# Optimization experiments

Measured on AMD Instinct MI355X. Metric: run time of the kernel, lower is better.

## Reference

```python
import jax, jax.numpy as jnp
import numpy as np

N_NODES = 50000
N_EDGES = 800000
H_DIM = 64
N_RELS = 8
N_BASES = 2
N_LAYERS = 2


def setup_inputs() -> dict:
    key = jax.random.key(0)
    ks = jax.random.split(key, 10)
    scale = 1.0 / np.sqrt(H_DIM)
    features = jax.random.normal(ks[0], (N_NODES, H_DIM), dtype=jnp.float32)
    src = jax.random.randint(ks[1], (N_EDGES,), 0, N_NODES, dtype=jnp.int32)
    dst = jax.random.randint(ks[2], (N_EDGES,), 0, N_NODES, dtype=jnp.int32)
    etype = jax.random.randint(ks[3], (N_EDGES,), 0, N_RELS, dtype=jnp.int32)
    # basis weights V: [L, B, H, H], coefficients comp: [L, R, B]
    V = jax.random.normal(ks[4], (N_LAYERS, N_BASES, H_DIM, H_DIM), dtype=jnp.float32) * scale
    comp = jax.random.normal(ks[5], (N_LAYERS, N_RELS, N_BASES), dtype=jnp.float32)
    loop_w = jax.random.normal(ks[6], (N_LAYERS, H_DIM, H_DIM), dtype=jnp.float32) * scale
    layer_bias = jnp.zeros((N_LAYERS, H_DIM), dtype=jnp.float32)
    fc_w = jax.random.normal(ks[7], (1, N_NODES * H_DIM), dtype=jnp.float32) * (1.0 / np.sqrt(N_NODES * H_DIM))
    fc_b = jnp.zeros((1,), dtype=jnp.float32)
    return {
        "features": features, "V": V, "comp": comp, "loop_w": loop_w,
        "layer_bias": layer_bias, "fc_w": fc_w, "fc_b": fc_b,
        "src": src, "dst": dst, "etype": etype,
    }


def reference(features, V, comp, loop_w, layer_bias, fc_w, fc_b, src, dst, etype):
    N, H = features.shape
    L = V.shape[0]
    x = features
    for l in range(L):
        # basis decomposition: project nodes through each basis first (N*B*H, cheap),
        # then mix per-edge with relation coefficients -> avoids per-edge [H,H] weights
        proj = jnp.einsum('ni,bio->nbo', x, V[l])          # [N, B, H]
        msg = jnp.einsum('eb,ebo->eo', comp[l][etype], proj[src])  # [E, H]
        agg = jax.ops.segment_sum(msg, dst, num_segments=N)        # [N, H]
        h = agg + x @ loop_w[l] + layer_bias[l]
        x = jax.nn.relu(h) if l < L - 1 else h
    flat = x.reshape(1, -1)                                # [1, N*H]
    return jax.nn.sigmoid(flat @ fc_w.T + fc_b)            # [1, 1]
```

## Files before the change

### kernel.cpp

```cpp
#include <hip/hip_runtime.h>
#include <hip/hip_bf16.h>
#include <math.h>

#define N_NODES 50000
#define N_EDGES 800000
#define HDIM 64

#define NBUCKET 98
#define BSHIFT  9
#define BCAP    10240

typedef short bf16x8 __attribute__((ext_vector_type(8)));
typedef float f32x4  __attribute__((ext_vector_type(4)));
typedef unsigned short ushort_t;

__device__ __forceinline__ ushort_t f2bf(float f) {
    __hip_bfloat16 b = __float2bfloat16(f);
    return *(ushort_t*)&b;
}
__device__ __forceinline__ void unpack8(uint4 u, float* f) {
    f[0] = __uint_as_float(u.x << 16); f[1] = __uint_as_float(u.x & 0xFFFF0000u);
    f[2] = __uint_as_float(u.y << 16); f[3] = __uint_as_float(u.y & 0xFFFF0000u);
    f[4] = __uint_as_float(u.z << 16); f[5] = __uint_as_float(u.z & 0xFFFF0000u);
    f[6] = __uint_as_float(u.w << 16); f[7] = __uint_as_float(u.w & 0xFFFF0000u);
}

__global__ __launch_bounds__(256) void prep_kernel(
    const float* __restrict__ features, ushort_t* __restrict__ x_bf,
    const float* __restrict__ V, const float* __restrict__ lw,
    ushort_t* __restrict__ Wt, int* __restrict__ bucketFill,
    float* __restrict__ scalar)
{
    const int b = blockIdx.x;
    const int t = threadIdx.x;
    if (b < 3125) {
        const int i = b * 256 + t;
        const float4 v = ((const float4*)features)[i];
        ushort4 o = { f2bf(v.x), f2bf(v.y), f2bf(v.z), f2bf(v.w) };
        *(ushort4*)&x_bf[(size_t)i * 4] = o;
    } else if (b < 3221) {
        const int e = (b - 3125) * 256 + t;
        const int l = e / 12288, r = e % 12288;
        const int n = r / 192, k = r % 192;
        const int sel = k >> 6, i = k & 63;
        const float val = (sel < 2) ? V[l * 8192 + sel * 4096 + i * 64 + n]
                                    : lw[l * 4096 + i * 64 + n];
        Wt[e] = f2bf(val);
    } else {
        if (t < NBUCKET) bucketFill[t] = 0;
        if (t == NBUCKET) scalar[0] = 0.0f;
    }
}

__global__ __launch_bounds__(256) void bucket_scatter(
    const int* __restrict__ src, const int* __restrict__ dst,
    const int* __restrict__ etype, int* __restrict__ bucketFill,
    unsigned int* __restrict__ buf)
{
    __shared__ int cnt[NBUCKET];
    __shared__ int base[NBUCKET];
    const int t = threadIdx.x;
    if (t < NBUCKET) cnt[t] = 0;
    __syncthreads();

    int rank[8], bkt[8];
    unsigned pay[8];
    bool valid[8];
#pragma unroll
    for (int k = 0; k < 8; ++k) {
        const int e = blockIdx.x * 2048 + k * 256 + t;
        valid[k] = (e < N_EDGES);
        if (valid[k]) {
            const int d = dst[e];
            const int b = d >> BSHIFT;
            bkt[k] = b;
            pay[k] = (unsigned)src[e] | ((unsigned)etype[e] << 16)
                   | ((unsigned)(d & 511) << 19);
            rank[k] = atomicAdd(&cnt[b], 1);
        }
    }
    __syncthreads();
    if (t < NBUCKET) base[t] = atomicAdd(&bucketFill[t], cnt[t]);
    __syncthreads();
#pragma unroll
    for (int k = 0; k < 8; ++k) {
        if (valid[k]) {
            const int pos = base[bkt[k]] + rank[k];
            if (pos < BCAP) buf[bkt[k] * BCAP + pos] = pay[k];
        }
    }
}

__global__ __launch_bounds__(256) void bucket_sort(
    const unsigned int* __restrict__ buf, const int* __restrict__ bucketFill,
    unsigned int* __restrict__ edges, int* __restrict__ row_ptr)
{
    __shared__ int hist[512];
    __shared__ int lscan[512];
    __shared__ int cnt2[512];
    __shared__ int sfill[128];
    __shared__ int sbase;
    const int b = blockIdx.x;
    const int t = threadIdx.x;

    hist[t] = 0; hist[t + 256] = 0;
    cnt2[t] = 0; cnt2[t + 256] = 0;
    if (t < NBUCKET) sfill[t] = bucketFill[t];
    else if (t < 128) sfill[t] = 0;
    __syncthreads();

    for (int off = 1; off < 128; off <<= 1) {
        int u = (t >= off && t < 128) ? sfill[t - off] : 0;
        __syncthreads();
        if (t < 128) sfill[t] += u;
        __syncthreads();
    }
    const int cntb = min(bucketFill[b], BCAP);
    if (t == 0) sbase = sfill[b] - bucketFill[b];
    __syncthreads();
    const int bb = sbase;

    for (int i = t; i < cntb; i += 256)
        atomicAdd(&hist[buf[b * BCAP + i] >> 19], 1);
    __syncthreads();

    if (t < 64) {
        int carry = 0;
        for (int c = 0; c < 8; ++c) {
            const int h = hist[c * 64 + t];
            int x = h;
#pragma unroll
            for (int off = 1; off < 64; off <<= 1) {
                int u = __shfl_up(x, off, 64);
                if (t >= off) x += u;
            }
            lscan[c * 64 + t] = carry + x - h;
            carry += __shfl(x, 63, 64);
        }
    }
    __syncthreads();

    const int n0 = b << BSHIFT;
    for (int i = t; i < 512; i += 256) {
        const int g = n0 + i;
        if (g < N_NODES) row_ptr[g] = bb + lscan[i];
    }
    if (b == NBUCKET - 1 && t == 0) row_ptr[N_NODES] = bb + cntb;

    for (int i = t; i < cntb; i += 256) {
        const unsigned p = buf[b * BCAP + i];
        const int d = p >> 19;
        const int r = atomicAdd(&cnt2[d], 1);
        edges[bb + lscan[d] + r] = p & 0x7FFFFu;
    }
}

__global__ __launch_bounds__(256) void aggregate_bf(
    const ushort_t* __restrict__ x,
    const unsigned int* __restrict__ edges,
    const int* __restrict__ row_ptr,
    const float* __restrict__ comp_l,
    ushort_t* __restrict__ y)
{
    const int lane = threadIdx.x & 63;
    const int n    = blockIdx.x * 4 + (threadIdx.x >> 6);
    const int g    = lane >> 3;
    const int fo   = lane & 7;

    const int beg = row_ptr[n];
    const int end = row_ptr[n + 1];

    float a0[8], a1[8];
#pragma unroll
    for (int i = 0; i < 8; ++i) { a0[i] = 0.f; a1[i] = 0.f; }

    for (int j = beg; j < end; j += 16) {
        const int j0 = j + g;
        const int j1 = j + 8 + g;
        const unsigned pk0 = edges[(j0 < end) ? j0 : (end - 1)];
        const unsigned pk1 = edges[(j1 < end) ? j1 : (end - 1)];
        float2 c0 = *(const float2*)&comp_l[(pk0 >> 16) * 2];
        float2 c1 = *(const float2*)&comp_l[(pk1 >> 16) * 2];
        if (j0 >= end) { c0.x = 0.f; c0.y = 0.f; }
        if (j1 >= end) { c1.x = 0.f; c1.y = 0.f; }
        const uint4 u0 = *(const uint4*)&x[(size_t)(pk0 & 0xFFFFu) * 64 + fo * 8];
        const uint4 u1 = *(const uint4*)&x[(size_t)(pk1 & 0xFFFFu) * 64 + fo * 8];
        float f0[8], f1[8];
        unpack8(u0, f0);
        unpack8(u1, f1);
#pragma unroll
        for (int i = 0; i < 8; ++i) {
            a0[i] = fmaf(c0.x, f0[i], a0[i]); a1[i] = fmaf(c0.y, f0[i], a1[i]);
            a0[i] = fmaf(c1.x, f1[i], a0[i]); a1[i] = fmaf(c1.y, f1[i], a1[i]);
        }
    }

#pragma unroll
    for (int m = 8; m <= 32; m <<= 1) {
#pragma unroll
        for (int i = 0; i < 8; ++i) {
            a0[i] += __shfl_xor(a0[i], m, 64);
            a1[i] += __shfl_xor(a1[i], m, 64);
        }
    }

    if (g == 0) {
        uint4 o0, o1;
        o0.x = (unsigned)f2bf(a0[0]) | ((unsigned)f2bf(a0[1]) << 16);
        o0.y = (unsigned)f2bf(a0[2]) | ((unsigned)f2bf(a0[3]) << 16);
        o0.z = (unsigned)f2bf(a0[4]) | ((unsigned)f2bf(a0[5]) << 16);
        o0.w = (unsigned)f2bf(a0[6]) | ((unsigned)f2bf(a0[7]) << 16);
        o1.x = (unsigned)f2bf(a1[0]) | ((unsigned)f2bf(a1[1]) << 16);
        o1.y = (unsigned)f2bf(a1[2]) | ((unsigned)f2bf(a1[3]) << 16);
        o1.z = (unsigned)f2bf(a1[4]) | ((unsigned)f2bf(a1[5]) << 16);
        o1.w = (unsigned)f2bf(a1[6]) | ((unsigned)f2bf(a1[7]) << 16);
        *(uint4*)&y[(size_t)n * 128 + fo * 8]      = o0;
        *(uint4*)&y[(size_t)n * 128 + 64 + fo * 8] = o1;
    }
}

template <bool FUSE>
__global__ __launch_bounds__(256) void mfma_transform(
    const ushort_t* __restrict__ y_bf,
    const ushort_t* __restrict__ x_bf,
    const ushort_t* __restrict__ Wt,
    const float* __restrict__ bias,
    const float* __restrict__ fcw,
    ushort_t* __restrict__ xout,
    float* __restrict__ scalar)
{
    __shared__ __align__(16) ushort_t su[64 * 200];
    __shared__ float sred[4];
    const int t = threadIdx.x;
    const int w = t >> 6;
    const int lane = t & 63;
    const int c16 = lane & 15;
    const int quad = lane >> 4;
    const int tile = blockIdx.x;

    bf16x8 wf[6];
#pragma unroll
    for (int kf = 0; kf < 6; ++kf)
        wf[kf] = *(const bf16x8*)&Wt[(w * 16 + c16) * 192 + kf * 32 + quad * 8];
    const float bv = bias[w * 16 + c16];

#pragma unroll
    for (int k = 0; k < 6; ++k) {
        const int cid = t + 256 * k;
        const int row = cid / 24;
        const int part = cid % 24;
        const int n = tile * 64 + row;
        uint4 v = {0u, 0u, 0u, 0u};
        if (n < N_NODES) {
            v = (part < 16) ? *(const uint4*)&y_bf[(size_t)n * 128 + part * 8]
                            : *(const uint4*)&x_bf[(size_t)n * 64 + (part - 16) * 8];
        }
        *(uint4*)&su[row * 200 + part * 8] = v;
    }
    __syncthreads();

    float fsum = 0.f;
#pragma unroll
    for (int mt = 0; mt < 4; ++mt) {
        f32x4 acc = {bv, bv, bv, bv};
#pragma unroll
        for (int kf = 0; kf < 6; ++kf) {
            const bf16x8 af =
                *(const bf16x8*)&su[(mt * 16 + c16) * 200 + kf * 32 + quad * 8];
            acc = __builtin_amdgcn_mfma_f32_16x16x32_bf16(af, wf[kf], acc, 0, 0, 0);
        }
        const int nodeb = tile * 64 + mt * 16 + quad * 4;
        if (FUSE) {
#pragma unroll
            for (int r = 0; r < 4; ++r) {
                const int n = nodeb + r;
                if (n < N_NODES)
                    fsum += acc[r] * fcw[(size_t)n * 64 + w * 16 + c16];
            }
        } else {
#pragma unroll
            for (int r = 0; r < 4; ++r) {
                const int n = nodeb + r;
                if (n < N_NODES)
                    xout[(size_t)n * 64 + w * 16 + c16] = f2bf(fmaxf(acc[r], 0.f));
            }
        }
    }

    if (FUSE) {
#pragma unroll
        for (int off = 32; off; off >>= 1) fsum += __shfl_down(fsum, off, 64);
        if (lane == 0) sred[w] = fsum;
        __syncthreads();
        if (t == 0) atomicAdd(scalar, sred[0] + sred[1] + sred[2] + sred[3]);
    }
}

__global__ void final_sigmoid(const float* __restrict__ scalar,
                              const float* __restrict__ fcb,
                              float* __restrict__ out)
{
    const float v = scalar[0] + fcb[0];
    out[0] = 1.0f / (1.0f + expf(-v));
}

extern "C" void kernel_launch(void* const* d_in, const int* in_sizes, int n_in,
                              void* d_out, int out_size, void* d_ws, size_t ws_size,
                              hipStream_t stream)
{
    const float* features = (const float*)d_in[0];
    const float* V        = (const float*)d_in[1];
    const float* comp     = (const float*)d_in[2];
    const float* loop_w   = (const float*)d_in[3];
    const float* bias     = (const float*)d_in[4];
    const float* fc_w     = (const float*)d_in[5];
    const float* fc_b     = (const float*)d_in[6];
    const int*   src      = (const int*)d_in[7];
    const int*   dst      = (const int*)d_in[8];
    const int*   etype    = (const int*)d_in[9];
    float* out = (float*)d_out;

    char* ws = (char*)d_ws;
    ushort_t*     y_bf    = (ushort_t*)(ws);
    ushort_t*     x_bf    = (ushort_t*)(ws + 12800000);
    ushort_t*     x1_bf   = (ushort_t*)(ws + 19200000);
    ushort_t*     Wt      = (ushort_t*)(ws + 25600000);
    float*        scalar  = (float*)   (ws + 25649152);
    int*          bucketFill = (int*)  (ws + 25649280);
    int*          row_ptr = (int*)     (ws + 25649792);
    unsigned int* edges   = (unsigned int*)(ws + 25849856);
    unsigned int* buf     = (unsigned int*)(ws + 29049856);

    const int aggBlocks = N_NODES / 4;
    const int mtBlocks  = (N_NODES + 63) / 64;
    const int k1Blocks  = (N_EDGES + 2047) / 2048;

    prep_kernel<<<3222, 256, 0, stream>>>(features, x_bf, V, loop_w, Wt,
                                          bucketFill, scalar);
    bucket_scatter<<<k1Blocks, 256, 0, stream>>>(src, dst, etype, bucketFill, buf);
    bucket_sort<<<NBUCKET, 256, 0, stream>>>(buf, bucketFill, edges, row_ptr);

    aggregate_bf<<<aggBlocks, 256, 0, stream>>>(x_bf, edges, row_ptr, comp, y_bf);
    mfma_transform<false><<<mtBlocks, 256, 0, stream>>>(
        y_bf, x_bf, Wt, bias, nullptr, x1_bf, nullptr);

    aggregate_bf<<<aggBlocks, 256, 0, stream>>>(x1_bf, edges, row_ptr, comp + 16, y_bf);
    mfma_transform<true><<<mtBlocks, 256, 0, stream>>>(
        y_bf, x1_bf, Wt + 12288, bias + 64, fc_w, nullptr, scalar);

    final_sigmoid<<<1, 1, 0, stream>>>(scalar, fc_b, out);
}
```

Baseline: 208.9 us.

## Assign one node per 8-lane group in aggregation and fuse sigmoid via last-block ticket

```diff
diff --git a/kernel.cpp b/kernel.cpp
--- a/kernel.cpp
+++ b/kernel.cpp
@@ -29,7 +29,7 @@
     const float* __restrict__ features, ushort_t* __restrict__ x_bf,
     const float* __restrict__ V, const float* __restrict__ lw,
     ushort_t* __restrict__ Wt, int* __restrict__ bucketFill,
-    float* __restrict__ scalar)
+    float* __restrict__ scalar, int* __restrict__ done)
 {
     const int b = blockIdx.x;
     const int t = threadIdx.x;
@@ -49,6 +49,7 @@
     } else {
         if (t < NBUCKET) bucketFill[t] = 0;
         if (t == NBUCKET) scalar[0] = 0.0f;
+        if (t == NBUCKET + 1) done[0] = 0;
     }
 }
 
@@ -163,48 +164,47 @@
     ushort_t* __restrict__ y)
 {
     const int lane = threadIdx.x & 63;
-    const int n    = blockIdx.x * 4 + (threadIdx.x >> 6);
+    const int wv   = threadIdx.x >> 6;
+    const int fo   = lane & 7;
     const int g    = lane >> 3;
-    const int fo   = lane & 7;
-
-    const int beg = row_ptr[n];
-    const int end = row_ptr[n + 1];
+    const int n    = blockIdx.x * 32 + wv * 8 + g;
+
+    int beg = 0, end = 0;
+    if (n < N_NODES) { beg = row_ptr[n]; end = row_ptr[n + 1]; }
 
     float a0[8], a1[8];
 #pragma unroll
     for (int i = 0; i < 8; ++i) { a0[i] = 0.f; a1[i] = 0.f; }
 
-    for (int j = beg; j < end; j += 16) {
-        const int j0 = j + g;
-        const int j1 = j + 8 + g;
-        const unsigned pk0 = edges[(j0 < end) ? j0 : (end - 1)];
-        const unsigned pk1 = edges[(j1 < end) ? j1 : (end - 1)];
-        float2 c0 = *(const float2*)&comp_l[(pk0 >> 16) * 2];
-        float2 c1 = *(const float2*)&comp_l[(pk1 >> 16) * 2];
-        if (j0 >= end) { c0.x = 0.f; c0.y = 0.f; }
-        if (j1 >= end) { c1.x = 0.f; c1.y = 0.f; }
-        const uint4 u0 = *(const uint4*)&x[(size_t)(pk0 & 0xFFFFu) * 64 + fo * 8];
-        const uint4 u1 = *(const uint4*)&x[(size_t)(pk1 & 0xFFFFu) * 64 + fo * 8];
-        float f0[8], f1[8];
-        unpack8(u0, f0);
-        unpack8(u1, f1);
-#pragma unroll
-        for (int i = 0; i < 8; ++i) {
-            a0[i] = fmaf(c0.x, f0[i], a0[i]); a1[i] = fmaf(c0.y, f0[i], a1[i]);
-            a0[i] = fmaf(c1.x, f1[i], a0[i]); a1[i] = fmaf(c1.y, f1[i], a1[i]);
-        }
-    }
-
-#pragma unroll
-    for (int m = 8; m <= 32; m <<= 1) {
-#pragma unroll
-        for (int i = 0; i < 8; ++i) {
-            a0[i] += __shfl_xor(a0[i], m, 64);
-            a1[i] += __shfl_xor(a1[i], m, 64);
-        }
-    }
-
-    if (g == 0) {
+    for (int j = beg; j < end; j += 4) {
+        unsigned pk[4];
+        float2 c[4];
+#pragma unroll
+        for (int k = 0; k < 4; ++k) {
+            const int jk = j + k;
+            const unsigned p = edges[(jk < end) ? jk : (end - 1)];
+            pk[k] = p;
+            float2 cc = *(const float2*)&comp_l[(p >> 16) * 2];
+            if (jk >= end) { cc.x = 0.f; cc.y = 0.f; }
+            c[k] = cc;
+        }
+        uint4 u[4];
+#pragma unroll
+        for (int k = 0; k < 4; ++k)
+            u[k] = *(const uint4*)&x[(size_t)(pk[k] & 0xFFFFu) * 64 + fo * 8];
+#pragma unroll
+        for (int k = 0; k < 4; ++k) {
+            float f[8];
+            unpack8(u[k], f);
+#pragma unroll
+            for (int i = 0; i < 8; ++i) {
+                a0[i] = fmaf(c[k].x, f[i], a0[i]);
+                a1[i] = fmaf(c[k].y, f[i], a1[i]);
+            }
+        }
+    }
+
+    if (n < N_NODES) {
         uint4 o0, o1;
         o0.x = (unsigned)f2bf(a0[0]) | ((unsigned)f2bf(a0[1]) << 16);
         o0.y = (unsigned)f2bf(a0[2]) | ((unsigned)f2bf(a0[3]) << 16);
@@ -227,7 +227,10 @@
     const float* __restrict__ bias,
     const float* __restrict__ fcw,
     ushort_t* __restrict__ xout,
-    float* __restrict__ scalar)
+    float* __restrict__ scalar,
+    const float* __restrict__ fcb,
+    int* __restrict__ done,
+    float* __restrict__ outp)
 {
     __shared__ __align__(16) ushort_t su[64 * 200];
     __shared__ float sred[4];
@@ -292,16 +295,16 @@
         for (int off = 32; off; off >>= 1) fsum += __shfl_down(fsum, off, 64);
         if (lane == 0) sred[w] = fsum;
         __syncthreads();
-        if (t == 0) atomicAdd(scalar, sred[0] + sred[1] + sred[2] + sred[3]);
-    }
-}
-
-__global__ void final_sigmoid(const float* __restrict__ scalar,
-                              const float* __restrict__ fcb,
-                              float* __restrict__ out)
-{
-    const float v = scalar[0] + fcb[0];
-    out[0] = 1.0f / (1.0f + expf(-v));
+        if (t == 0) {
+            atomicAdd(scalar, sred[0] + sred[1] + sred[2] + sred[3]);
+            __threadfence();
+            const int ticket = atomicAdd(done, 1);
+            if (ticket == (int)gridDim.x - 1) {
+                const float v = atomicAdd(scalar, 0.0f) + fcb[0];
+                outp[0] = 1.0f / (1.0f + expf(-v));
+            }
+        }
+    }
 }
 
 extern "C" void kernel_launch(void* const* d_in, const int* in_sizes, int n_in,
@@ -326,27 +329,26 @@
     ushort_t*     x1_bf   = (ushort_t*)(ws + 19200000);
     ushort_t*     Wt      = (ushort_t*)(ws + 25600000);
     float*        scalar  = (float*)   (ws + 25649152);
+    int*          done    = (int*)     (ws + 25649160);
     int*          bucketFill = (int*)  (ws + 25649280);
     int*          row_ptr = (int*)     (ws + 25649792);
     unsigned int* edges   = (unsigned int*)(ws + 25849856);
     unsigned int* buf     = (unsigned int*)(ws + 29049856);
 
-    const int aggBlocks = N_NODES / 4;
+    const int aggBlocks = (N_NODES + 31) / 32;
     const int mtBlocks  = (N_NODES + 63) / 64;
     const int k1Blocks  = (N_EDGES + 2047) / 2048;
 
     prep_kernel<<<3222, 256, 0, stream>>>(features, x_bf, V, loop_w, Wt,
-                                          bucketFill, scalar);
+                                          bucketFill, scalar, done);
     bucket_scatter<<<k1Blocks, 256, 0, stream>>>(src, dst, etype, bucketFill, buf);
     bucket_sort<<<NBUCKET, 256, 0, stream>>>(buf, bucketFill, edges, row_ptr);
 
     aggregate_bf<<<aggBlocks, 256, 0, stream>>>(x_bf, edges, row_ptr, comp, y_bf);
     mfma_transform<false><<<mtBlocks, 256, 0, stream>>>(
-        y_bf, x_bf, Wt, bias, nullptr, x1_bf, nullptr);
+        y_bf, x_bf, Wt, bias, nullptr, x1_bf, nullptr, nullptr, nullptr, nullptr);
 
     aggregate_bf<<<aggBlocks, 256, 0, stream>>>(x1_bf, edges, row_ptr, comp + 16, y_bf);
     mfma_transform<true><<<mtBlocks, 256, 0, stream>>>(
-        y_bf, x1_bf, Wt + 12288, bias + 64, fc_w, nullptr, scalar);
-
-    final_sigmoid<<<1, 1, 0, stream>>>(scalar, fc_b, out);
-}
+        y_bf, x1_bf, Wt + 12288, bias + 64, fc_w, nullptr, scalar, fc_b, done, out);
+}
```

New measurement: 199.9 us. 4.3% less time.
